# Performance work log

Measured on AMD Instinct MI355X. Metric: run time of the kernel, lower is better.

The kernel has to match this reference:

```python
import jax, jax.numpy as jnp
import numpy as np

BATCH, GROUPS, ARITY, OUT_DIM = 1024, 512, 4, 64


def _high_order_act(X, params):
    # X: [B, G, K]; params: [G, 2**K, D]
    A_ind = jnp.argsort(X, axis=2)                                   # [B,G,K] int
    A_sort = jnp.take_along_axis(X, A_ind, axis=2)                   # sorted values
    # barycentric-style coefficients: smallest value, then successive gaps
    coef = jnp.concatenate(
        [A_sort[:, :, :1], A_sort[:, :, 1:] - A_sort[:, :, :-1]], axis=2
    )                                                                 # [B,G,K]
    # reversed cumulative sum of 2**A_ind -> vertex index into 2**K table
    pow2 = jnp.left_shift(jnp.int32(1), A_ind.astype(jnp.int32))      # [B,G,K]
    idx = jnp.flip(jnp.cumsum(jnp.flip(pow2, axis=2), axis=2), axis=2)  # [B,G,K]
    G = params.shape[0]
    g_idx = jnp.arange(G)[None, :, None]                              # [1,G,1]
    pg = params[g_idx, idx]                                           # [B,G,K,D] gather
    return jnp.einsum('bgk,bgkd->bgd', coef, pg)                      # [B,G,D]


def setup_inputs() -> dict:
    key = jax.random.key(0)
    k1, k2 = jax.random.split(key)
    X = jax.random.normal(k1, (BATCH, GROUPS, ARITY), dtype=jnp.float32)
    params = jax.random.normal(k2, (GROUPS, 2 ** ARITY, OUT_DIM), dtype=jnp.float32)
    return {"X": X, "params": params}


def reference(X, params):
    return _high_order_act(X, params)
```

## Files before the change

kernel.cpp:

```cpp
#include <hip/hip_runtime.h>

#define BATCH   1024
#define GROUPS  512
#define OUT_DIM 64

#define ROW_WORDS 68

__global__ __launch_bounds__(256) void hoact_kernel(
    const float4* __restrict__ X4,
    const float4* __restrict__ P4,
    float4*       __restrict__ O4)
{
    __shared__ float tbl[16 * ROW_WORDS];

    const int g     = blockIdx.x >> 3;
    const int chunk = blockIdx.x & 7;
    const int b0    = chunk * 128;
    const int tid   = threadIdx.x;

    {
        const float4 v = P4[g * 256 + tid];
        const int row = tid >> 4, c4 = tid & 15;
        *(float4*)&tbl[row * ROW_WORDS + c4 * 4] = v;
    }

    const int t       = tid & 7;
    const int bl_base = tid >> 3;

    float4 xv[4];
#pragma unroll
    for (int p = 0; p < 4; ++p) {
        const int b = b0 + p * 32 + bl_base;
        xv[p] = X4[b * GROUPS + g];
    }

    __syncthreads();

#pragma unroll
    for (int p = 0; p < 4; ++p) {
        const int b = b0 + p * 32 + bl_base;
        const float4 x = xv[p];

        float v0 = __uint_as_float((__float_as_uint(x.x) & ~3u) | 0u);
        float v1 = __uint_as_float((__float_as_uint(x.y) & ~3u) | 1u);
        float v2 = __uint_as_float((__float_as_uint(x.z) & ~3u) | 2u);
        float v3 = __uint_as_float((__float_as_uint(x.w) & ~3u) | 3u);

#define CSWAP(a, b_)                                 \
        {                                            \
            const float lo = fminf((a), (b_));       \
            const float hi = fmaxf((a), (b_));       \
            (a) = lo; (b_) = hi;                     \
        }
        CSWAP(v0, v1);
        CSWAP(v2, v3);
        CSWAP(v0, v2);
        CSWAP(v1, v3);
        CSWAP(v1, v2);
#undef CSWAP

        const int i1 = __float_as_uint(v1) & 3;
        const int i2 = __float_as_uint(v2) & 3;
        const int i3 = __float_as_uint(v3) & 3;

        const float c0 = v0;
        const float c1 = v1 - v0;
        const float c2 = v2 - v1;
        const float c3 = v3 - v2;

        const int e3 = 1 << i3;
        const int e2 = e3 + (1 << i2);
        const int e1 = e2 + (1 << i1);

        const float4 p0a = *(const float4*)&tbl[15 * ROW_WORDS + t * 4];
        const float4 p0b = *(const float4*)&tbl[15 * ROW_WORDS + (t + 8) * 4];
        const float4 p1a = *(const float4*)&tbl[e1 * ROW_WORDS + t * 4];
        const float4 p1b = *(const float4*)&tbl[e1 * ROW_WORDS + (t + 8) * 4];
        const float4 p2a = *(const float4*)&tbl[e2 * ROW_WORDS + t * 4];
        const float4 p2b = *(const float4*)&tbl[e2 * ROW_WORDS + (t + 8) * 4];
        const float4 p3a = *(const float4*)&tbl[e3 * ROW_WORDS + t * 4];
        const float4 p3b = *(const float4*)&tbl[e3 * ROW_WORDS + (t + 8) * 4];

        float4 oa, ob;
        oa.x = c0 * p0a.x + c1 * p1a.x + c2 * p2a.x + c3 * p3a.x;
        oa.y = c0 * p0a.y + c1 * p1a.y + c2 * p2a.y + c3 * p3a.y;
        oa.z = c0 * p0a.z + c1 * p1a.z + c2 * p2a.z + c3 * p3a.z;
        oa.w = c0 * p0a.w + c1 * p1a.w + c2 * p2a.w + c3 * p3a.w;
        ob.x = c0 * p0b.x + c1 * p1b.x + c2 * p2b.x + c3 * p3b.x;
        ob.y = c0 * p0b.y + c1 * p1b.y + c2 * p2b.y + c3 * p3b.y;
        ob.z = c0 * p0b.z + c1 * p1b.z + c2 * p2b.z + c3 * p3b.z;
        ob.w = c0 * p0b.w + c1 * p1b.w + c2 * p2b.w + c3 * p3b.w;

        const int o_idx = b * (GROUPS * 16) + g * 16 + t;
        O4[o_idx]     = oa;
        O4[o_idx + 8] = ob;
    }
}

extern "C" void kernel_launch(void* const* d_in, const int* in_sizes, int n_in,
                              void* d_out, int out_size, void* d_ws, size_t ws_size,
                              hipStream_t stream) {
    const float4* X4 = (const float4*)d_in[0];
    const float4* P4 = (const float4*)d_in[1];
    float4*       O4 = (float4*)d_out;

    const int grid = GROUPS * 8;
    hipLaunchKernelGGL(hoact_kernel, dim3(grid), dim3(256), 0, stream,
                       X4, P4, O4);
}
```

Before: 146.1 us.

## Tile four groups per block so each wavefront stores contiguous 1KB output rows

```diff
diff --git a/kernel.cpp b/kernel.cpp
--- a/kernel.cpp
+++ b/kernel.cpp
@@ -3,42 +3,48 @@
 #define BATCH   1024
 #define GROUPS  512
 #define OUT_DIM 64
+#define G_TILE  4
+#define B_TILE  32
 
-#define ROW_WORDS 68
+typedef float f32x4 __attribute__((ext_vector_type(4)));
 
 __global__ __launch_bounds__(256) void hoact_kernel(
     const float4* __restrict__ X4,
     const float4* __restrict__ P4,
     float4*       __restrict__ O4)
 {
-    __shared__ float tbl[16 * ROW_WORDS];
+    __shared__ float tbl[G_TILE * 16 * 64];
 
-    const int g     = blockIdx.x >> 3;
-    const int chunk = blockIdx.x & 7;
-    const int b0    = chunk * 128;
-    const int tid   = threadIdx.x;
+    const int gtile  = blockIdx.x & 127;
+    const int bchunk = blockIdx.x >> 7;
+    const int g0     = gtile * G_TILE;
+    const int b0     = bchunk * B_TILE;
+    const int tid    = threadIdx.x;
 
-    {
-        const float4 v = P4[g * 256 + tid];
-        const int row = tid >> 4, c4 = tid & 15;
-        *(float4*)&tbl[row * ROW_WORDS + c4 * 4] = v;
+#pragma unroll
+    for (int k = 0; k < 4; ++k) {
+        const int q = tid + k * 256;
+        *(f32x4*)&tbl[q * 4] = *(const f32x4*)&P4[g0 * 256 + q];
     }
 
-    const int t       = tid & 7;
-    const int bl_base = tid >> 3;
+    const int w        = tid >> 6;
+    const int gl       = (tid >> 4) & 3;
+    const int c4       = tid & 15;
+    const int lane64   = tid & 63;
+    const int lds_base = gl * 1024;
 
-    float4 xv[4];
+    float4 xv[8];
 #pragma unroll
-    for (int p = 0; p < 4; ++p) {
-        const int b = b0 + p * 32 + bl_base;
-        xv[p] = X4[b * GROUPS + g];
+    for (int p = 0; p < 8; ++p) {
+        const int b = b0 + p * 4 + w;
+        xv[p] = X4[b * GROUPS + g0 + gl];
     }
 
     __syncthreads();
 
 #pragma unroll
-    for (int p = 0; p < 4; ++p) {
-        const int b = b0 + p * 32 + bl_base;
+    for (int p = 0; p < 8; ++p) {
+        const int b = b0 + p * 4 + w;
         const float4 x = xv[p];
 
         float v0 = __uint_as_float((__float_as_uint(x.x) & ~3u) | 0u);
@@ -72,28 +78,19 @@
         const int e2 = e3 + (1 << i2);
         const int e1 = e2 + (1 << i1);
 
-        const float4 p0a = *(const float4*)&tbl[15 * ROW_WORDS + t * 4];
-        const float4 p0b = *(const float4*)&tbl[15 * ROW_WORDS + (t + 8) * 4];
-        const float4 p1a = *(const float4*)&tbl[e1 * ROW_WORDS + t * 4];
-        const float4 p1b = *(const float4*)&tbl[e1 * ROW_WORDS + (t + 8) * 4];
-        const float4 p2a = *(const float4*)&tbl[e2 * ROW_WORDS + t * 4];
-        const float4 p2b = *(const float4*)&tbl[e2 * ROW_WORDS + (t + 8) * 4];
-        const float4 p3a = *(const float4*)&tbl[e3 * ROW_WORDS + t * 4];
-        const float4 p3b = *(const float4*)&tbl[e3 * ROW_WORDS + (t + 8) * 4];
+        const f32x4 p0 = *(const f32x4*)&tbl[lds_base + 15 * 64 + c4 * 4];
+        const f32x4 p1 = *(const f32x4*)&tbl[lds_base + e1 * 64 + c4 * 4];
+        const f32x4 p2 = *(const f32x4*)&tbl[lds_base + e2 * 64 + c4 * 4];
+        const f32x4 p3 = *(const f32x4*)&tbl[lds_base + e3 * 64 + c4 * 4];
 
-        float4 oa, ob;
-        oa.x = c0 * p0a.x + c1 * p1a.x + c2 * p2a.x + c3 * p3a.x;
-        oa.y = c0 * p0a.y + c1 * p1a.y + c2 * p2a.y + c3 * p3a.y;
-        oa.z = c0 * p0a.z + c1 * p1a.z + c2 * p2a.z + c3 * p3a.z;
-        oa.w = c0 * p0a.w + c1 * p1a.w + c2 * p2a.w + c3 * p3a.w;
-        ob.x = c0 * p0b.x + c1 * p1b.x + c2 * p2b.x + c3 * p3b.x;
-        ob.y = c0 * p0b.y + c1 * p1b.y + c2 * p2b.y + c3 * p3b.y;
-        ob.z = c0 * p0b.z + c1 * p1b.z + c2 * p2b.z + c3 * p3b.z;
-        ob.w = c0 * p0b.w + c1 * p1b.w + c2 * p2b.w + c3 * p3b.w;
+        f32x4 o;
+        o.x = c0 * p0.x + c1 * p1.x + c2 * p2.x + c3 * p3.x;
+        o.y = c0 * p0.y + c1 * p1.y + c2 * p2.y + c3 * p3.y;
+        o.z = c0 * p0.z + c1 * p1.z + c2 * p2.z + c3 * p3.z;
+        o.w = c0 * p0.w + c1 * p1.w + c2 * p2.w + c3 * p3.w;
 
-        const int o_idx = b * (GROUPS * 16) + g * 16 + t;
-        O4[o_idx]     = oa;
-        O4[o_idx + 8] = ob;
+        const int o_idx = b * (GROUPS * 16) + gtile * 64 + lane64;
+        __builtin_nontemporal_store(o, (f32x4*)&O4[o_idx]);
     }
 }
 
@@ -104,7 +101,7 @@
     const float4* P4 = (const float4*)d_in[1];
     float4*       O4 = (float4*)d_out;
 
-    const int grid = GROUPS * 8;
+    const int grid = (GROUPS / G_TILE) * (BATCH / B_TILE);
     hipLaunchKernelGGL(hoact_kernel, dim3(grid), dim3(256), 0, stream,
                        X4, P4, O4);
 }
```

New measurement: 153.7 us. +5.2%, slower.

## Process full batch per group block with rolling X prefetch and unpadded table

Applied to the files above, without the earlier changes.

```diff
diff --git a/kernel.cpp b/kernel.cpp
--- a/kernel.cpp
+++ b/kernel.cpp
@@ -2,44 +2,44 @@
 
 #define BATCH   1024
 #define GROUPS  512
-#define OUT_DIM 64
 
-#define ROW_WORDS 68
+typedef float f32x4 __attribute__((ext_vector_type(4)));
 
 __global__ __launch_bounds__(256) void hoact_kernel(
     const float4* __restrict__ X4,
     const float4* __restrict__ P4,
     float4*       __restrict__ O4)
 {
-    __shared__ float tbl[16 * ROW_WORDS];
+    __shared__ float tbl[16 * 64];
 
-    const int g     = blockIdx.x >> 3;
-    const int chunk = blockIdx.x & 7;
-    const int b0    = chunk * 128;
-    const int tid   = threadIdx.x;
+    const int g   = (blockIdx.x & 7) * 64 + (blockIdx.x >> 3);
+    const int tid = threadIdx.x;
 
     {
         const float4 v = P4[g * 256 + tid];
-        const int row = tid >> 4, c4 = tid & 15;
-        *(float4*)&tbl[row * ROW_WORDS + c4 * 4] = v;
+        *(float4*)&tbl[tid << 2] = v;
     }
 
-    const int t       = tid & 7;
-    const int bl_base = tid >> 3;
+    const int t  = tid & 7;
+    const int bl = tid >> 3;
 
     float4 xv[4];
 #pragma unroll
-    for (int p = 0; p < 4; ++p) {
-        const int b = b0 + p * 32 + bl_base;
-        xv[p] = X4[b * GROUPS + g];
-    }
+    for (int p = 0; p < 4; ++p)
+        xv[p] = X4[(p * 32 + bl) * GROUPS + g];
 
     __syncthreads();
 
-#pragma unroll
-    for (int p = 0; p < 4; ++p) {
-        const int b = b0 + p * 32 + bl_base;
-        const float4 x = xv[p];
+    const f32x4 p0a = *(const f32x4*)&tbl[15 * 64 + t * 4];
+    const f32x4 p0b = *(const f32x4*)&tbl[15 * 64 + (t + 8) * 4];
+
+#pragma unroll 4
+    for (int p = 0; p < 32; ++p) {
+        const int b = p * 32 + bl;
+        const float4 x = xv[p & 3];
+
+        if (p < 28)
+            xv[p & 3] = X4[((p + 4) * 32 + bl) * GROUPS + g];
 
         float v0 = __uint_as_float((__float_as_uint(x.x) & ~3u) | 0u);
         float v1 = __uint_as_float((__float_as_uint(x.y) & ~3u) | 1u);
@@ -72,14 +72,12 @@
         const int e2 = e3 + (1 << i2);
         const int e1 = e2 + (1 << i1);
 
-        const float4 p0a = *(const float4*)&tbl[15 * ROW_WORDS + t * 4];
-        const float4 p0b = *(const float4*)&tbl[15 * ROW_WORDS + (t + 8) * 4];
-        const float4 p1a = *(const float4*)&tbl[e1 * ROW_WORDS + t * 4];
-        const float4 p1b = *(const float4*)&tbl[e1 * ROW_WORDS + (t + 8) * 4];
-        const float4 p2a = *(const float4*)&tbl[e2 * ROW_WORDS + t * 4];
-        const float4 p2b = *(const float4*)&tbl[e2 * ROW_WORDS + (t + 8) * 4];
-        const float4 p3a = *(const float4*)&tbl[e3 * ROW_WORDS + t * 4];
-        const float4 p3b = *(const float4*)&tbl[e3 * ROW_WORDS + (t + 8) * 4];
+        const f32x4 p1a = *(const f32x4*)&tbl[(e1 << 6) + t * 4];
+        const f32x4 p1b = *(const f32x4*)&tbl[(e1 << 6) + (t + 8) * 4];
+        const f32x4 p2a = *(const f32x4*)&tbl[(e2 << 6) + t * 4];
+        const f32x4 p2b = *(const f32x4*)&tbl[(e2 << 6) + (t + 8) * 4];
+        const f32x4 p3a = *(const f32x4*)&tbl[(e3 << 6) + t * 4];
+        const f32x4 p3b = *(const f32x4*)&tbl[(e3 << 6) + (t + 8) * 4];
 
         float4 oa, ob;
         oa.x = c0 * p0a.x + c1 * p1a.x + c2 * p2a.x + c3 * p3a.x;
@@ -104,7 +102,7 @@
     const float4* P4 = (const float4*)d_in[1];
     float4*       O4 = (float4*)d_out;
 
-    const int grid = GROUPS * 8;
+    const int grid = 512;
     hipLaunchKernelGGL(hoact_kernel, dim3(grid), dim3(256), 0, stream,
                        X4, P4, O4);
 }
```

New measurement: 148.5 us. Within noise of the previous version (+1.7%).
